# Performance work log

Hardware: AMD Instinct MI355X
Metric: run time of the kernel (lower is better)

The kernel has to match this reference:

```python
import jax, jax.numpy as jnp
import numpy as np

N, E, G = 8192, 65536, 64
DIMS = [(74, 2048), (2048, 1024), (1024, 512), (512, 512)]
EDGE_DIM = 21


def setup_inputs() -> dict:
    key = jax.random.key(0)
    ks = jax.random.split(key, 64)
    x = jax.random.uniform(ks[0], (N, 10), jnp.float32)
    x = x.at[:, 0].set(jax.random.randint(ks[1], (N,), 1, 119).astype(jnp.float32))
    x = x.at[:, 9].set(jax.random.randint(ks[2], (N,), 0, 2).astype(jnp.float32))
    edge_index = jax.random.randint(ks[3], (2, E), 0, N, dtype=jnp.int32)
    edge_attr = jax.random.uniform(ks[4], (E, 4), jnp.float32)
    edge_attr = edge_attr.at[:, 0].set(jax.random.randint(ks[5], (E,), 1, 22).astype(jnp.float32))
    edge_attr = edge_attr.at[:, 2].set(jax.random.randint(ks[6], (E,), 0, 2).astype(jnp.float32))
    edge_attr = edge_attr.at[:, 3].set(jax.random.randint(ks[7], (E,), 0, 2).astype(jnp.float32))
    batch = jnp.sort(jax.random.randint(ks[8], (N,), 0, G, dtype=jnp.int32))
    atom_emb = (jax.random.normal(ks[9], (119, 64), jnp.float32) * 0.1).at[0].set(0.0)
    bond_emb = (jax.random.normal(ks[10], (22, 16), jnp.float32) * 0.1).at[0].set(0.0)
    bool_emb = (jax.random.normal(ks[11], (3, 2), jnp.float32) * 0.1).at[2].set(0.0)
    inp = dict(x=x, edge_attr=edge_attr, atom_emb=atom_emb, bond_emb=bond_emb,
               bool_emb=bool_emb, edge_index=edge_index, batch=batch)
    ki = 12
    for li, (din, dout) in enumerate(DIMS, start=1):
        s = 1.0 / np.sqrt(din)
        inp[f"Wl{li}"] = jax.random.normal(ks[ki], (din, dout), jnp.float32) * s; ki += 1
        inp[f"bl{li}"] = jnp.zeros((dout,), jnp.float32)
        inp[f"Wr{li}"] = jax.random.normal(ks[ki], (din, dout), jnp.float32) * s; ki += 1
        inp[f"br{li}"] = jnp.zeros((dout,), jnp.float32)
        inp[f"We{li}"] = jax.random.normal(ks[ki], (EDGE_DIM, dout), jnp.float32) * (1.0 / np.sqrt(EDGE_DIM)); ki += 1
        inp[f"att{li}"] = jax.random.normal(ks[ki], (dout,), jnp.float32) * (1.0 / np.sqrt(dout)); ki += 1
        inp[f"b{li}"] = jnp.zeros((dout,), jnp.float32)
    return inp


def _gatv2(h, src, tgt, ea, Wl, bl, Wr, br, We, att, b):
    # PyG GATv2Conv, heads=1, negative_slope=0.2 (self-loops already appended)
    n = h.shape[0]
    xl = h @ Wl + bl                           # source transform  [N, C]
    xr = h @ Wr + br                           # target transform  [N, C]
    m = xl[src] + xr[tgt] + ea @ We            # per-edge message  [E', C]
    a = jax.nn.leaky_relu(m, 0.2) @ att        # attention logits  [E']
    amax = jax.ops.segment_max(a, tgt, num_segments=n)
    ex = jnp.exp(a - amax[tgt])                # edge softmax over incoming edges
    denom = jax.ops.segment_sum(ex, tgt, num_segments=n)
    alpha = ex / denom[tgt]
    return jax.ops.segment_sum(alpha[:, None] * xl[src], tgt, num_segments=n) + b


def _forward(x, edge_attr, atom_emb, bond_emb, bool_emb, params, edge_index, batch):
    n = x.shape[0]
    # feature encoding: [atom_emb(64) | 8 float feats | bool_emb(2)] -> 74
    h = jnp.concatenate([atom_emb[x[:, 0].astype(jnp.int32)], x[:, 1:9],
                         bool_emb[x[:, 9].astype(jnp.int32)]], axis=1)
    # edge encoding: [bond_emb(16) | 1 float | bool_emb(2) | bool_emb(2)] -> 21
    ea = jnp.concatenate([bond_emb[edge_attr[:, 0].astype(jnp.int32)], edge_attr[:, 1:2],
                          bool_emb[edge_attr[:, 2].astype(jnp.int32)],
                          bool_emb[edge_attr[:, 3].astype(jnp.int32)]], axis=1)
    src, tgt = edge_index[0], edge_index[1]
    # add_self_loops with fill_value='mean': self-loop attr = mean of incoming edge attrs
    cnt = jax.ops.segment_sum(jnp.ones(src.shape, h.dtype), tgt, num_segments=n)
    loop_attr = jax.ops.segment_sum(ea, tgt, num_segments=n) / jnp.maximum(cnt, 1.0)[:, None]
    loop = jnp.arange(n, dtype=src.dtype)
    src = jnp.concatenate([src, loop])
    tgt = jnp.concatenate([tgt, loop])
    ea = jnp.concatenate([ea, loop_attr], axis=0)
    for p in params:  # 4 GATv2 layers + ReLU (dropout = identity in eval)
        h = jax.nn.relu(_gatv2(h, src, tgt, ea, *p))
    gcnt = jax.ops.segment_sum(jnp.ones(batch.shape, h.dtype), batch, num_segments=G)
    return jax.ops.segment_sum(h, batch, num_segments=G) / jnp.maximum(gcnt, 1.0)[:, None]


def reference(x, edge_attr, atom_emb, bond_emb, bool_emb,
              Wl1, bl1, Wr1, br1, We1, att1, b1,
              Wl2, bl2, Wr2, br2, We2, att2, b2,
              Wl3, bl3, Wr3, br3, We3, att3, b3,
              Wl4, bl4, Wr4, br4, We4, att4, b4,
              edge_index, batch):
    params = [(Wl1, bl1, Wr1, br1, We1, att1, b1),
              (Wl2, bl2, Wr2, br2, We2, att2, b2),
              (Wl3, bl3, Wr3, br3, We3, att3, b3),
              (Wl4, bl4, Wr4, br4, We4, att4, b4)]
    return _forward(x, edge_attr, atom_emb, bond_emb, bool_emb, params, edge_index, batch)
```

## Files before the change

### kernel.cpp

```cpp
#include <hip/hip_runtime.h>
#include <hip/hip_bf16.h>

#define N_NODES 8192
#define N_EDGES 65536
#define EP (N_EDGES + N_NODES)
#define N_GROUPS 64
#define DEGCAP 64
#define EDGE_B 4

typedef _Float16 f16_t;
typedef f16_t  f16x8  __attribute__((ext_vector_type(8)));
typedef f16_t  h2     __attribute__((ext_vector_type(2)));
typedef f16_t  h4     __attribute__((ext_vector_type(4)));
typedef float  f32x4  __attribute__((ext_vector_type(4)));
typedef unsigned u32x2 __attribute__((ext_vector_type(2)));

__device__ __forceinline__ float lrelu(float v){ return v > 0.f ? v : 0.2f*v; }

__device__ __forceinline__ void gload_lds16(const void* g, void* l){
  typedef __attribute__((address_space(1))) const void gvoid_t;
  typedef __attribute__((address_space(3))) void lvoid_t;
  __builtin_amdgcn_global_load_lds((gvoid_t*)g, (lvoid_t*)l, 16, 0, 0);
}

__device__ __forceinline__ unsigned pkh2(float a, float b){
  union{h2 h; unsigned u;} c; c.h[0] = (f16_t)a; c.h[1] = (f16_t)b; return c.u;
}
__device__ __forceinline__ h2 as_h2(unsigned u){ union{unsigned x; h2 h;} c; c.x = u; return c.h; }
__device__ __forceinline__ unsigned pkh(f16_t a, f16_t b){
  unsigned short ua = *(unsigned short*)&a, ub = *(unsigned short*)&b;
  return (unsigned)ua | ((unsigned)ub << 16);
}

#if __has_builtin(__builtin_amdgcn_fdot2)
#define FDOT2(a,b,c) __builtin_amdgcn_fdot2((a),(b),(c),false)
#else
#define FDOT2(a,b,c) ((c) + (float)(a)[0]*(float)(b)[0] + (float)(a)[1]*(float)(b)[1])
#endif

__global__ void k_encode_nodes(const float* __restrict__ x, const float* __restrict__ atom_emb,
                               const float* __restrict__ bool_emb, float* __restrict__ h){
  int idx = blockIdx.x*blockDim.x + threadIdx.x;
  if (idx >= N_NODES*74) return;
  int n = idx / 74, c = idx % 74;
  float v;
  if (c < 64)      { int ai = (int)x[n*10+0]; v = atom_emb[ai*64 + c]; }
  else if (c < 72) { v = x[n*10 + 1 + (c-64)]; }
  else             { int bi = (int)x[n*10+9]; v = bool_emb[bi*2 + (c-72)]; }
  h[n*74 + c] = v;
}

__global__ void k_deg(const int* __restrict__ ei, int* __restrict__ deg){
  int e = blockIdx.x*blockDim.x + threadIdx.x;
  if (e >= N_EDGES) return;
  atomicAdd(&deg[ei[N_EDGES + e]], 1);
}

__global__ __launch_bounds__(1024) void k_scan(const int* __restrict__ deg, int* __restrict__ rowptr){
  __shared__ int buf[1024];
  int t = threadIdx.x;
  int loc[8]; int s = 0;
  #pragma unroll
  for (int i=0;i<8;++i){ loc[i]=s; s += deg[t*8+i] + 1; }
  buf[t] = s; __syncthreads();
  for (int off=1; off<1024; off<<=1){
    int v = (t>=off) ? buf[t-off] : 0; __syncthreads();
    buf[t] += v; __syncthreads();
  }
  int base = buf[t] - s;
  #pragma unroll
  for (int i=0;i<8;++i) rowptr[t*8+i] = base + loc[i];
  if (t==1023) rowptr[8192] = buf[1023];
}

__global__ void k_fill(const int* __restrict__ ei, const int* __restrict__ rowptr,
                       int* __restrict__ fillpos, int* __restrict__ csr_src,
                       int* __restrict__ posE){
  int e = blockIdx.x*blockDim.x + threadIdx.x;
  if (e >= EP) return;
  int s, tg;
  if (e < N_EDGES){ s = ei[e]; tg = ei[N_EDGES+e]; }
  else            { s = tg = e - N_EDGES; }
  int pos = rowptr[tg] + atomicAdd(&fillpos[tg], 1);
  csr_src[pos] = s; posE[e] = pos;
}

__global__ void k_dhist(const int* __restrict__ rowptr, int* __restrict__ hist){
  int n = blockIdx.x*blockDim.x + threadIdx.x;
  if (n >= N_NODES) return;
  int d = rowptr[n+1] - rowptr[n];
  if (d > DEGCAP) d = DEGCAP;
  atomicAdd(&hist[d], 1);
}
__global__ void k_dscan(const int* __restrict__ hist, int* __restrict__ boff){
  if (threadIdx.x || blockIdx.x) return;
  int acc = 0;
  for (int d = DEGCAP; d >= 0; --d){ boff[d] = acc; acc += hist[d]; }
}
__global__ void k_dscatter(const int* __restrict__ rowptr, const int* __restrict__ boff,
                           int* __restrict__ bcnt, int* __restrict__ perm){
  int n = blockIdx.x*blockDim.x + threadIdx.x;
  if (n >= N_NODES) return;
  int d = rowptr[n+1] - rowptr[n];
  if (d > DEGCAP) d = DEGCAP;
  perm[boff[d] + atomicAdd(&bcnt[d], 1)] = n;
}

__global__ void k_encode_edges(const float* __restrict__ edge_attr, const float* __restrict__ bond_emb,
                               const float* __restrict__ bool_emb, const int* __restrict__ posE,
                               unsigned* __restrict__ ea_pk){
  int e = blockIdx.x*blockDim.x + threadIdx.x;
  if (e >= N_EDGES) return;
  float a0 = edge_attr[e*4+0], a1 = edge_attr[e*4+1];
  float a2 = edge_attr[e*4+2], a3 = edge_attr[e*4+3];
  int bi = (int)a0, b2 = (int)a2, b3 = (int)a3;
  int pos = posE[e];
  float v[22];
  #pragma unroll
  for (int j=0;j<16;++j) v[j] = bond_emb[bi*16+j];
  v[16] = a1;
  v[17] = bool_emb[b2*2+0]; v[18] = bool_emb[b2*2+1];
  v[19] = bool_emb[b3*2+0]; v[20] = bool_emb[b3*2+1];
  v[21] = 0.f;
  #pragma unroll
  for (int j=0;j<11;++j) ea_pk[(size_t)pos*12 + j] = pkh2(v[2*j], v[2*j+1]);
  ea_pk[(size_t)pos*12 + 11] = 0u;
}

__global__ void k_loopsum(const float* __restrict__ edge_attr, const float* __restrict__ bond_emb,
                          const float* __restrict__ bool_emb, const int* __restrict__ ei,
                          float* __restrict__ loopsum){
  int e = blockIdx.x*blockDim.x + threadIdx.x;
  if (e >= N_EDGES) return;
  float a0 = edge_attr[e*4+0], a1 = edge_attr[e*4+1];
  float a2 = edge_attr[e*4+2], a3 = edge_attr[e*4+3];
  int bi = (int)a0, b2 = (int)a2, b3 = (int)a3;
  int tg = ei[N_EDGES + e];
  float v[21];
  #pragma unroll
  for (int j=0;j<16;++j) v[j] = bond_emb[bi*16+j];
  v[16] = a1;
  v[17] = bool_emb[b2*2+0]; v[18] = bool_emb[b2*2+1];
  v[19] = bool_emb[b3*2+0]; v[20] = bool_emb[b3*2+1];
  #pragma unroll
  for (int j=0;j<21;++j) atomicAdd(&loopsum[tg*21+j], v[j]);
}

__global__ void k_loop_attr(const float* __restrict__ loopsum, const int* __restrict__ deg,
                            const int* __restrict__ posE, unsigned* __restrict__ ea_pk){
  int n = blockIdx.x*blockDim.x + threadIdx.x;
  if (n >= N_NODES) return;
  float c = (float)deg[n]; if (c < 1.f) c = 1.f;
  float inv = 1.f / c;
  int pos = posE[N_EDGES + n];
  float v[22];
  #pragma unroll
  for (int j=0;j<21;++j) v[j] = loopsum[n*21+j] * inv;
  v[21] = 0.f;
  #pragma unroll
  for (int j=0;j<11;++j) ea_pk[(size_t)pos*12 + j] = pkh2(v[2*j], v[2*j+1]);
  ea_pk[(size_t)pos*12 + 11] = 0u;
}

__global__ void k_goff(const int* __restrict__ batch, int* __restrict__ goff){
  int n = blockIdx.x*blockDim.x + threadIdx.x;
  if (n >= N_NODES) return;
  int b = batch[n];
  if (n == 0){ for (int g=0; g<=b; ++g) goff[g] = 0; }
  else { int bp = batch[n-1]; for (int g=bp+1; g<=b; ++g) goff[g] = n; }
  if (n == N_NODES-1){ for (int g=b+1; g<=N_GROUPS; ++g) goff[g] = N_NODES; }
}

__global__ void k_splitA(const float* __restrict__ A, f16_t* __restrict__ Ah,
                         f16_t* __restrict__ Al, int K, int Kp){
  int idx = blockIdx.x*blockDim.x + threadIdx.x;
  if (idx >= N_NODES*Kp) return;
  int k = idx % Kp;
  int n = idx / Kp;
  float v = (k < K) ? A[(size_t)n*K + k] : 0.f;
  f16_t hi = (f16_t)v;
  f16_t lo = (f16_t)(v - (float)hi);
  Ah[idx] = hi; Al[idx] = lo;
}

__global__ void k_splitW2(const float* __restrict__ Wl, const float* __restrict__ Wr,
                          f16_t* __restrict__ W2, int K, int Kp, int Nc){
  int idx = blockIdx.x*blockDim.x + threadIdx.x;
  if (idx >= 2*Nc*Kp) return;
  int k = idx % Kp;
  int n = idx / Kp;
  const float* W = (n < Nc) ? Wl : Wr;
  int nn = (n < Nc) ? n : n - Nc;
  float v = (k < K) ? W[(size_t)k*Nc + nn] : 0.f;
  W2[idx] = (f16_t)v;
}

__global__ void k_packWe(const float* __restrict__ We, unsigned* __restrict__ We_pk, int C){
  int c = blockIdx.x*blockDim.x + threadIdx.x;
  if (c >= C) return;
  #pragma unroll
  for (int j=0;j<10;++j)
    We_pk[(size_t)j*C + c] = pkh2(We[(size_t)(2*j)*C + c], We[(size_t)(2*j+1)*C + c]);
  We_pk[(size_t)10*C + c] = pkh2(We[(size_t)20*C + c], 0.f);
}

#define BM 128
#define BN 128
#define BK 64
__global__ __launch_bounds__(256) void k_gemm2_mfma(
    const f16_t* __restrict__ Ah, const f16_t* __restrict__ Al,
    const f16_t* __restrict__ W2,
    const float* __restrict__ bl, const float* __restrict__ br,
    f16_t* __restrict__ XLh, float* __restrict__ XR,
    int Kp, int Chalf)
{
  __shared__ __align__(16) f16_t sA[BM*BK];
  __shared__ __align__(16) f16_t sB[BN*BK];
  int t = threadIdx.x;
  int lane = t & 63;
  int w = t >> 6;
  int wr = w >> 1, wc = w & 1;

  int lin = blockIdx.y * gridDim.x + blockIdx.x;
  int nwg = gridDim.x * gridDim.y;
  int qd = nwg >> 3, rm = nwg & 7;
  int xcd = lin & 7, sub = lin >> 3;
  int work = (xcd < rm ? xcd*(qd+1) : rm*(qd+1) + (xcd-rm)*qd) + sub;
  int bn = (work % gridDim.x) * BN;
  int bm = (work / gridDim.x) * BM;

  f32x4 acc[4][4] = {};

  int srow = t >> 3;
  int scol = (t & 7) * 8;

  for (int seg = 0; seg < 2; ++seg){
    const f16_t* As = seg ? Al : Ah;
    for (int k0 = 0; k0 < Kp; k0 += BK){
      #pragma unroll
      for (int i = 0; i < 4; ++i){
        int row = srow + i*32;
        gload_lds16(As + (size_t)(bm + row)*Kp + k0 + scol, (char*)sA + (t + i*256)*16);
        gload_lds16(W2 + (size_t)(bn + row)*Kp + k0 + scol, (char*)sB + (t + i*256)*16);
      }
      __syncthreads();
      #pragma unroll
      for (int kk = 0; kk < BK; kk += 32){
        f16x8 af[4], bfr[4];
        int ko = kk + (lane >> 4)*8;
        #pragma unroll
        for (int m=0;m<4;++m)
          af[m] = *(const f16x8*)&sA[(wr*64 + m*16 + (lane&15))*BK + ko];
        #pragma unroll
        for (int n=0;n<4;++n)
          bfr[n] = *(const f16x8*)&sB[(wc*64 + n*16 + (lane&15))*BK + ko];
        #pragma unroll
        for (int m=0;m<4;++m)
          #pragma unroll
          for (int n=0;n<4;++n)
            acc[m][n] = __builtin_amdgcn_mfma_f32_16x16x32_f16(af[m], bfr[n], acc[m][n], 0, 0, 0);
      }
      __syncthreads();
    }
  }

  bool left = (bn < Chalf);
  int cadj = left ? 0 : Chalf;
  const float* bias = left ? bl : br;
  int r0 = bm + wr*64 + ((lane>>4)<<2);
  int c0 = bn + wc*64 + (lane&15);
  #pragma unroll
  for (int n=0;n<4;++n){
    int col = c0 + n*16 - cadj;
    float bv = bias[col];
    #pragma unroll
    for (int m=0;m<4;++m){
      #pragma unroll
      for (int j=0;j<4;++j){
        size_t idx = (size_t)(r0 + m*16 + j)*Chalf + col;
        float v = acc[m][n][j] + bv;
        if (left) XLh[idx] = (f16_t)v;
        else      XR[idx]  = v;
      }
    }
  }
}

__global__ __launch_bounds__(256) void k_edge_fused(
    const f16_t* __restrict__ XLh,
    const float* __restrict__ XR,
    const unsigned* __restrict__ ea_pk, const unsigned* __restrict__ We_pk,
    const float* __restrict__ att, const float* __restrict__ bias,
    const int* __restrict__ rowptr, const int* __restrict__ csr_src,
    const int* __restrict__ perm,
    f16_t* __restrict__ AhN, f16_t* __restrict__ AlN,
    float* __restrict__ houtF, int C)
{
  __shared__ float sPart[4][DEGCAP];
  __shared__ float sAl[DEGCAP];
  __shared__ int   sSrc[DEGCAP];
  int t = threadIdx.x;
  int lane = t & 63, q = t >> 6;
  int n = perm[blockIdx.x];
  int p0 = rowptr[n];
  int deg = rowptr[n+1] - p0;
  if (deg > DEGCAP) deg = DEGCAP;
  int p0s = __builtin_amdgcn_readfirstlane(p0);

  if (q == 0 && lane < deg) sSrc[lane] = csr_src[p0 + lane];
  __syncthreads();

  float lpart = 0.f;
  for (int g = 0; g < deg; g += EDGE_B){
    unsigned earr[EDGE_B][11];
    int sidx[EDGE_B];
    #pragma unroll
    for (int i=0;i<EDGE_B;++i){
      int qq = (g+i < deg) ? (g+i) : 0;
      sidx[i] = sSrc[qq];
      const unsigned* ep = ea_pk + (size_t)(p0s+qq)*12;
      #pragma unroll
      for (int j=0;j<11;++j) earr[i][j] = ep[j];
    }
    float acc[EDGE_B] = {0.f,0.f,0.f,0.f};
    for (int c0 = q*128; c0 < C; c0 += 512){
      int c = c0 + 2*lane;
      u32x2 wpk[11];
      #pragma unroll
      for (int j=0;j<11;++j) wpk[j] = *(const u32x2*)&We_pk[(size_t)j*C + c];
      float2 xr2 = *(const float2*)&XR[(size_t)n*C + c];
      float2 at2 = *(const float2*)&att[c];
      #pragma unroll
      for (int i=0;i<EDGE_B;++i){
        if (g+i < deg){
          h2 xl2 = as_h2(*(const unsigned*)(XLh + (size_t)sidx[i]*C + c));
          float m0 = (float)xl2[0] + xr2.x;
          float m1 = (float)xl2[1] + xr2.y;
          #pragma unroll
          for (int j=0;j<11;++j){
            h2 e = as_h2(earr[i][j]);
            m0 = FDOT2(e, as_h2(wpk[j][0]), m0);
            m1 = FDOT2(e, as_h2(wpk[j][1]), m1);
          }
          acc[i] += lrelu(m0)*at2.x + lrelu(m1)*at2.y;
        }
      }
    }
    #pragma unroll
    for (int i=0;i<EDGE_B;++i){
      if (g+i < deg){
        float v = acc[i];
        #pragma unroll
        for (int off=32; off; off>>=1) v += __shfl_xor(v, off);
        if (lane == g+i) lpart = v;
      }
    }
  }

  sPart[q][lane] = lpart;
  __syncthreads();
  if (q == 0){
    float tot = (lane < deg) ? (sPart[0][lane] + sPart[1][lane] +
                                sPart[2][lane] + sPart[3][lane]) : -1e30f;
    float mx = tot;
    #pragma unroll
    for (int off=32; off; off>>=1) mx = fmaxf(mx, __shfl_xor(mx, off));
    float ex = (lane < deg) ? __expf(tot - mx) : 0.f;
    float sm = ex;
    #pragma unroll
    for (int off=32; off; off>>=1) sm += __shfl_xor(sm, off);
    sAl[lane] = ex / sm;
  }
  __syncthreads();

  int cbase = q*(C>>2), cend = cbase + (C>>2);
  for (int c0 = cbase + 4*lane; c0 < cend; c0 += 256){
    float a0 = bias[c0], a1 = bias[c0+1], a2 = bias[c0+2], a3 = bias[c0+3];
    for (int p = 0; p < deg; ++p){
      float al = sAl[p];
      int s = sSrc[p];
      h4 hh = *(const h4*)(XLh + (size_t)s*C + c0);
      a0 += al * (float)hh[0];
      a1 += al * (float)hh[1];
      a2 += al * (float)hh[2];
      a3 += al * (float)hh[3];
    }
    float r0 = fmaxf(a0, 0.f), r1 = fmaxf(a1, 0.f);
    float r2 = fmaxf(a2, 0.f), r3 = fmaxf(a3, 0.f);
    if (houtF){
      f32x4 rv = {r0, r1, r2, r3};
      *(f32x4*)&houtF[(size_t)n*C + c0] = rv;
    } else {
      f16_t h0 = (f16_t)r0, h1 = (f16_t)r1, h2v = (f16_t)r2, h3 = (f16_t)r3;
      f16_t l0 = (f16_t)(r0 - (float)h0), l1 = (f16_t)(r1 - (float)h1);
      f16_t l2 = (f16_t)(r2 - (float)h2v), l3 = (f16_t)(r3 - (float)h3);
      u32x2 wh = {pkh(h0, h1), pkh(h2v, h3)};
      u32x2 wl = {pkh(l0, l1), pkh(l2, l3)};
      *(u32x2*)&AhN[(size_t)n*C + c0] = wh;
      *(u32x2*)&AlN[(size_t)n*C + c0] = wl;
    }
  }
}

__global__ void k_pool(const float* __restrict__ h, const int* __restrict__ goff,
                       float* __restrict__ out){
  int g = blockIdx.x >> 1;
  int c = ((blockIdx.x & 1) * 256) + threadIdx.x;
  int n0 = goff[g], n1 = goff[g+1];
  float s = 0.f;
  for (int n=n0;n<n1;++n) s += h[(size_t)n*512 + c];
  float cf = (float)(n1-n0); if (cf < 1.f) cf = 1.f;
  out[g*512 + c] = s / cf;
}

extern "C" void kernel_launch(void* const* d_in, const int* in_sizes, int n_in,
                              void* d_out, int out_size, void* d_ws, size_t ws_size,
                              hipStream_t stream) {
  (void)in_sizes; (void)n_in; (void)out_size; (void)ws_size;
  const float* x         = (const float*)d_in[0];
  const float* edge_attr = (const float*)d_in[1];
  const float* atom_emb  = (const float*)d_in[2];
  const float* bond_emb  = (const float*)d_in[3];
  const float* bool_emb  = (const float*)d_in[4];
  const int*   ei        = (const int*)d_in[5];
  const int*   batch     = (const int*)d_in[6];

  struct Layer { const float *Wl,*bl,*Wr,*br,*We,*att,*b; int Cin,Cout,Kp; };
  const int dims[5] = {74, 2048, 1024, 512, 512};
  const int kpad[4] = {128, 2048, 1024, 512};
  Layer L[4];
  for (int i=0;i<4;++i){
    const int o = 7 + i*7;
    L[i] = { (const float*)d_in[o+0], (const float*)d_in[o+1], (const float*)d_in[o+2],
             (const float*)d_in[o+3], (const float*)d_in[o+4], (const float*)d_in[o+5],
             (const float*)d_in[o+6], dims[i], dims[i+1], kpad[i] };
  }

  char* ws = (char*)d_ws;
  size_t off = 0;
  auto alloc = [&](size_t bytes)->void*{ void* p = ws + off; off += (bytes + 255) & ~(size_t)255; return p; };
  f16_t* p0Ah = (f16_t*)alloc((size_t)N_NODES*1024*2);
  f16_t* p0Al = (f16_t*)alloc((size_t)N_NODES*1024*2);
  f16_t* p1Ah = (f16_t*)alloc((size_t)N_NODES*2048*2);
  f16_t* p1Al = (f16_t*)alloc((size_t)N_NODES*2048*2);
  f16_t* XLh  = (f16_t*)alloc((size_t)N_NODES*2048*2);
  float* XR   = (float*)alloc((size_t)N_NODES*2048*4);
  float* hfin = (float*)alloc((size_t)N_NODES*512*4);
  float* h0   = (float*)alloc((size_t)N_NODES*74*4);
  f16_t* W2b  = (f16_t*)alloc((size_t)2*1024*2048*2);
  unsigned* We_pk = (unsigned*)alloc((size_t)11*2048*4);
  unsigned* ea_pk = (unsigned*)alloc((size_t)EP*12*4);
  float* loopsum = (float*)alloc((size_t)N_NODES*21*4);
  int*   deg     = (int*)alloc((size_t)N_NODES*4);
  int*   rowptr  = (int*)alloc((size_t)(N_NODES+1)*4);
  int*   fillpos = (int*)alloc((size_t)N_NODES*4);
  int*   csr_src = (int*)alloc((size_t)EP*4);
  int*   posE    = (int*)alloc((size_t)EP*4);
  int*   goff    = (int*)alloc((size_t)(N_GROUPS+1)*4);
  int*   dhist   = (int*)alloc((size_t)(DEGCAP+1)*4);
  int*   dboff   = (int*)alloc((size_t)(DEGCAP+1)*4);
  int*   dbcnt   = (int*)alloc((size_t)(DEGCAP+1)*4);
  int*   perm    = (int*)alloc((size_t)N_NODES*4);

  hipMemsetAsync(loopsum, 0, (size_t)N_NODES*21*4, stream);
  hipMemsetAsync(deg,     0, (size_t)N_NODES*4, stream);
  hipMemsetAsync(fillpos, 0, (size_t)N_NODES*4, stream);
  hipMemsetAsync(dhist,   0, (size_t)(DEGCAP+1)*4, stream);
  hipMemsetAsync(dbcnt,   0, (size_t)(DEGCAP+1)*4, stream);

  k_encode_nodes<<<(N_NODES*74 + 255)/256, 256, 0, stream>>>(x, atom_emb, bool_emb, h0);
  k_deg<<<N_EDGES/256, 256, 0, stream>>>(ei, deg);
  k_scan<<<1, 1024, 0, stream>>>(deg, rowptr);
  k_fill<<<(EP + 255)/256, 256, 0, stream>>>(ei, rowptr, fillpos, csr_src, posE);
  k_dhist<<<N_NODES/256, 256, 0, stream>>>(rowptr, dhist);
  k_dscan<<<1, 64, 0, stream>>>(dhist, dboff);
  k_dscatter<<<N_NODES/256, 256, 0, stream>>>(rowptr, dboff, dbcnt, perm);
  k_encode_edges<<<N_EDGES/256, 256, 0, stream>>>(edge_attr, bond_emb, bool_emb, posE, ea_pk);
  k_loopsum<<<N_EDGES/256, 256, 0, stream>>>(edge_attr, bond_emb, bool_emb, ei, loopsum);
  k_loop_attr<<<(N_NODES + 255)/256, 256, 0, stream>>>(loopsum, deg, posE, ea_pk);
  k_goff<<<N_NODES/256, 256, 0, stream>>>(batch, goff);

  k_splitA<<<((size_t)N_NODES*128 + 255)/256, 256, 0, stream>>>(h0, p0Ah, p0Al, 74, 128);

  f16_t* pairAh[2] = { p0Ah, p1Ah };
  f16_t* pairAl[2] = { p0Al, p1Al };
  for (int li=0; li<4; ++li){
    int cur = li & 1, nxt = cur ^ 1;
    int C = L[li].Cout, Kp = L[li].Kp;
    dim3 ggrid(2*C/BN, N_NODES/BM);

    k_splitW2<<<((size_t)2*C*Kp + 255)/256, 256, 0, stream>>>(L[li].Wl, L[li].Wr, W2b,
                                                              L[li].Cin, Kp, C);
    k_gemm2_mfma<<<ggrid, 256, 0, stream>>>(pairAh[cur], pairAl[cur], W2b,
                                            L[li].bl, L[li].br, XLh, XR, Kp, C);

    k_packWe<<<(C + 255)/256, 256, 0, stream>>>(L[li].We, We_pk, C);

    if (li < 3)
      k_edge_fused<<<N_NODES, 256, 0, stream>>>(XLh, XR, ea_pk, We_pk, L[li].att,
                                                L[li].b, rowptr, csr_src, perm,
                                                pairAh[nxt], pairAl[nxt],
                                                (float*)nullptr, C);
    else
      k_edge_fused<<<N_NODES, 256, 0, stream>>>(XLh, XR, ea_pk, We_pk, L[li].att,
                                                L[li].b, rowptr, csr_src, perm,
                                                (f16_t*)nullptr, (f16_t*)nullptr,
                                                hfin, C);
  }

  k_pool<<<N_GROUPS*2, 256, 0, stream>>>(hfin, goff, (float*)d_out);
}
```

Baseline: 1.026 ms.

## Fuse hi/lo A segments into one K loop sharing B tiles; drop XCD remap

The GEMM used to run two full K passes, one for the high half of the split-fp16 activations and one for the low half, reloading the weight tile each time. It now loads both A halves and a single B tile per K step into LDS and issues MFMAs for both from the same B fragments. This halves B traffic and the number of barriers. It also removes the XCD-aware block-index remapping in favour of plain blockIdx mapping, which may hurt L2 locality. LDS use grows by one tile, which may reduce occupancy.

```diff
diff --git a/kernel.cpp b/kernel.cpp
--- a/kernel.cpp
+++ b/kernel.cpp
@@ -214,54 +214,52 @@
     f16_t* __restrict__ XLh, float* __restrict__ XR,
     int Kp, int Chalf)
 {
-  __shared__ __align__(16) f16_t sA[BM*BK];
-  __shared__ __align__(16) f16_t sB[BN*BK];
+  __shared__ __align__(16) f16_t sAh[BM*BK];
+  __shared__ __align__(16) f16_t sAl[BM*BK];
+  __shared__ __align__(16) f16_t sB [BN*BK];
   int t = threadIdx.x;
   int lane = t & 63;
   int w = t >> 6;
   int wr = w >> 1, wc = w & 1;
-
-  int lin = blockIdx.y * gridDim.x + blockIdx.x;
-  int nwg = gridDim.x * gridDim.y;
-  int qd = nwg >> 3, rm = nwg & 7;
-  int xcd = lin & 7, sub = lin >> 3;
-  int work = (xcd < rm ? xcd*(qd+1) : rm*(qd+1) + (xcd-rm)*qd) + sub;
-  int bn = (work % gridDim.x) * BN;
-  int bm = (work / gridDim.x) * BM;
+  int bm = blockIdx.y * BM, bn = blockIdx.x * BN;
 
   f32x4 acc[4][4] = {};
 
   int srow = t >> 3;
   int scol = (t & 7) * 8;
 
-  for (int seg = 0; seg < 2; ++seg){
-    const f16_t* As = seg ? Al : Ah;
-    for (int k0 = 0; k0 < Kp; k0 += BK){
-      #pragma unroll
-      for (int i = 0; i < 4; ++i){
-        int row = srow + i*32;
-        gload_lds16(As + (size_t)(bm + row)*Kp + k0 + scol, (char*)sA + (t + i*256)*16);
-        gload_lds16(W2 + (size_t)(bn + row)*Kp + k0 + scol, (char*)sB + (t + i*256)*16);
-      }
-      __syncthreads();
-      #pragma unroll
-      for (int kk = 0; kk < BK; kk += 32){
-        f16x8 af[4], bfr[4];
-        int ko = kk + (lane >> 4)*8;
-        #pragma unroll
-        for (int m=0;m<4;++m)
-          af[m] = *(const f16x8*)&sA[(wr*64 + m*16 + (lane&15))*BK + ko];
+  for (int k0 = 0; k0 < Kp; k0 += BK){
+    #pragma unroll
+    for (int i = 0; i < 4; ++i){
+      int row = srow + i*32;
+      gload_lds16(Ah + (size_t)(bm + row)*Kp + k0 + scol, (char*)sAh + (t + i*256)*16);
+      gload_lds16(Al + (size_t)(bm + row)*Kp + k0 + scol, (char*)sAl + (t + i*256)*16);
+      gload_lds16(W2 + (size_t)(bn + row)*Kp + k0 + scol, (char*)sB  + (t + i*256)*16);
+    }
+    __syncthreads();
+    #pragma unroll
+    for (int kk = 0; kk < BK; kk += 32){
+      int ko = kk + (lane >> 4)*8;
+      f16x8 bfr[4];
+      #pragma unroll
+      for (int n=0;n<4;++n)
+        bfr[n] = *(const f16x8*)&sB[(wc*64 + n*16 + (lane&15))*BK + ko];
+      #pragma unroll
+      for (int m=0;m<4;++m){
+        f16x8 ah = *(const f16x8*)&sAh[(wr*64 + m*16 + (lane&15))*BK + ko];
         #pragma unroll
         for (int n=0;n<4;++n)
-          bfr[n] = *(const f16x8*)&sB[(wc*64 + n*16 + (lane&15))*BK + ko];
+          acc[m][n] = __builtin_amdgcn_mfma_f32_16x16x32_f16(ah, bfr[n], acc[m][n], 0, 0, 0);
+      }
+      #pragma unroll
+      for (int m=0;m<4;++m){
+        f16x8 al = *(const f16x8*)&sAl[(wr*64 + m*16 + (lane&15))*BK + ko];
         #pragma unroll
-        for (int m=0;m<4;++m)
-          #pragma unroll
-          for (int n=0;n<4;++n)
-            acc[m][n] = __builtin_amdgcn_mfma_f32_16x16x32_f16(af[m], bfr[n], acc[m][n], 0, 0, 0);
+        for (int n=0;n<4;++n)
+          acc[m][n] = __builtin_amdgcn_mfma_f32_16x16x32_f16(al, bfr[n], acc[m][n], 0, 0, 0);
       }
-      __syncthreads();
-    }
+    }
+    __syncthreads();
   }
 
   bool left = (bn < Chalf);
```

New measurement: 961.3 us. -6.3%, faster.
